# Performance work log

Hardware: AMD Instinct MI355X
Metric: run time of the kernel (lower is better)

The kernel has to match this reference:

```python
import jax, jax.numpy as jnp
import numpy as np

B, S, D, H = 4, 2048, 1024, 16
HD = D // H

def setup_inputs() -> dict:
    key = jax.random.key(0)
    ks = jax.random.split(key, 12)
    std = 1.0 / np.sqrt(D)
    inp = {
        'query': jax.random.normal(ks[0], (B, S, D), jnp.float32),
        'key':   jax.random.normal(ks[1], (B, S, D), jnp.float32),
        'value': jax.random.normal(ks[2], (B, S, D), jnp.float32),
        'mask':  jnp.tril(jnp.ones((S, S), jnp.int32))[None, None, :, :],  # [1,1,S,S] causal
        'Wq': jax.random.uniform(ks[3], (D, D), jnp.float32, -std, std),
        'bq': jax.random.uniform(ks[4], (D,), jnp.float32, -std, std),
        'Wk': jax.random.uniform(ks[5], (D, D), jnp.float32, -std, std),
        'bk': jax.random.uniform(ks[6], (D,), jnp.float32, -std, std),
        'Wv': jax.random.uniform(ks[7], (D, D), jnp.float32, -std, std),
        'bv': jax.random.uniform(ks[8], (D,), jnp.float32, -std, std),
        'Wo': jax.random.uniform(ks[9], (D, D), jnp.float32, -std, std),
        'bo': jax.random.uniform(ks[10], (D,), jnp.float32, -std, std),
    }
    return inp

def _split_heads(x, W, b):
    # torch Linear: x @ W.T + b ; then [B,S,H,HD] -> [B,H,S,HD]
    y = jnp.einsum('bsd,ed->bse', x, W) + b
    return y.reshape(x.shape[0], -1, H, HD).transpose(0, 2, 1, 3)

def reference(query, key, value, mask, Wq, bq, Wk, bk, Wv, bv, Wo, bo):
    q = _split_heads(query, Wq, bq)   # [B,H,S,HD]
    k = _split_heads(key,   Wk, bk)
    v = _split_heads(value, Wv, bv)
    logits = jnp.einsum('bhqd,bhkd->bhqk', q, k) / np.sqrt(HD)  # [B,H,S,S]
    logits = jnp.where(mask == 0, jnp.float32(-1e9), logits)
    attn = jax.nn.softmax(logits, axis=-1)
    out = jnp.einsum('bhqk,bhkd->bhqd', attn, v)               # [B,H,S,HD]
    out = out.transpose(0, 2, 1, 3).reshape(query.shape[0], -1, D)
    return jnp.einsum('bsd,ed->bse', out, Wo) + bo
```

## Files before the change

kernel.cpp:

```cpp
#include <hip/hip_runtime.h>
#include <hip/hip_bf16.h>


#define SLEN 2048
#define DMOD 1024

typedef __attribute__((ext_vector_type(8))) short s16x8;
typedef __attribute__((ext_vector_type(4))) float f32x4;

__device__ __forceinline__ unsigned short f2bf(float f) {
    union { __hip_bfloat16 h; unsigned short u; } cv;
    cv.h = __float2bfloat16(f);
    return cv.u;
}
__device__ __forceinline__ unsigned cvtpk(float a, float b) {
    unsigned r;
    asm("v_cvt_pk_bf16_f32 %0, %1, %2" : "=v"(r) : "v"(a), "v"(b));
    return r;
}
__device__ __forceinline__ void gload_lds16(const void* g, void* l) {
    __builtin_amdgcn_global_load_lds(
        (const __attribute__((address_space(1))) void*)g,
        (__attribute__((address_space(3))) void*)l, 16, 0, 0);
}

__global__ __launch_bounds__(256) void convert_w(
    const float* __restrict__ wq, const float* __restrict__ wk,
    const float* __restrict__ wv, const float* __restrict__ wo,
    unsigned short* __restrict__ dst)
{
    const int bid = blockIdx.x, tid = threadIdx.x;
    const int w = bid >> 7;
    const float* src = (w == 0) ? wq : (w == 1) ? wk : (w == 2) ? wv : wo;
    unsigned short* d = dst + (size_t)w * 1048576;
    const size_t off = (size_t)(bid & 127) * 8192;
#pragma unroll
    for (int i = 0; i < 8; ++i) {
        const size_t e = off + (size_t)(i * 256 + tid) * 4;
        float4 x = *reinterpret_cast<const float4*>(&src[e]);
        uint2 u;
        u.x = cvtpk(x.x, x.y);
        u.y = cvtpk(x.z, x.w);
        *reinterpret_cast<uint2*>(&d[e]) = u;
    }
}

template<int MODE>
__global__ __launch_bounds__(256, 2) void gemm_qkv(
    const float* __restrict__ A, const unsigned short* __restrict__ W,
    const float* __restrict__ bias, unsigned short* __restrict__ outp,
    float oscale)
{
    __shared__ unsigned short Asm[2][8192];
    __shared__ unsigned short Bsm[2][8192];

    const int tid  = threadIdx.x;
    const int lane = tid & 63, wid = tid >> 6;
    const int l15 = lane & 15, lhi = lane >> 4;

    const int flat = blockIdx.x;
    const int logical = (flat & 7) * 64 + (flat >> 3);
    const int m0 = (logical >> 3) * 128, n0 = (logical & 7) * 128;
    const int wr = wid >> 1, wc = wid & 1;

    int soff[4];
    const float* aptc[4];
#pragma unroll
    for (int i = 0; i < 4; ++i) {
        const int f = i * 256 + tid;
        const int srow = f >> 3, sg = f & 7;
        soff[i] = srow * 128 + ((sg ^ (srow & 7)) * 16);
        aptc[i] = A + (size_t)(m0 + srow) * 1024 + sg * 8;
    }
    const int wsrow = lane >> 3;
    const int wsgr  = (lane & 7) ^ wsrow;
    const unsigned short* bpt = W + (size_t)(n0 + wid * 8 + wsrow) * 1024 + wsgr * 8;

    int aoff[2][4], boff[2][4];
#pragma unroll
    for (int kk = 0; kk < 2; ++kk)
#pragma unroll
        for (int i = 0; i < 4; ++i) {
            const int s = ((4 * kk + lhi) ^ (l15 & 7)) * 16;
            aoff[kk][i] = (wr * 64 + i * 16 + l15) * 128 + s;
            boff[kk][i] = (wc * 64 + i * 16 + l15) * 128 + s;
        }

    f32x4 acc[4][4];
#pragma unroll
    for (int i = 0; i < 4; ++i)
#pragma unroll
        for (int j = 0; j < 4; ++j) acc[i][j] = (f32x4)0.f;

    float4 awE[8], awO[8];

    auto loadTo = [&](float4 (&aw)[8], int k0) {
#pragma unroll
        for (int i = 0; i < 4; ++i) {
            aw[2 * i]     = *reinterpret_cast<const float4*>(aptc[i] + k0);
            aw[2 * i + 1] = *reinterpret_cast<const float4*>(aptc[i] + k0 + 4);
        }
    };
    auto writeFrom = [&](float4 (&aw)[8], int bsel) {
#pragma unroll
        for (int i = 0; i < 4; ++i) {
            uint4 u;
            u.x = cvtpk(aw[2 * i].x,     aw[2 * i].y);
            u.y = cvtpk(aw[2 * i].z,     aw[2 * i].w);
            u.z = cvtpk(aw[2 * i + 1].x, aw[2 * i + 1].y);
            u.w = cvtpk(aw[2 * i + 1].z, aw[2 * i + 1].w);
            *reinterpret_cast<uint4*>((char*)&Asm[bsel][0] + soff[i]) = u;
        }
    };
    auto stageW = [&](int bsel) {
        char* bd = (char*)Bsm + bsel * 16384 + wid * 1024;
#pragma unroll
        for (int i = 0; i < 4; ++i)
            gload_lds16(bpt + i * 32768, bd + i * 4096);
        bpt += 64;
    };
    auto mfmaPhase = [&](const char* AB, const char* BB) {
#pragma unroll
        for (int kk = 0; kk < 2; ++kk) {
            s16x8 af[4], bfv[4];
#pragma unroll
            for (int i = 0; i < 4; ++i) af[i]  = *reinterpret_cast<const s16x8*>(AB + aoff[kk][i]);
#pragma unroll
            for (int j = 0; j < 4; ++j) bfv[j] = *reinterpret_cast<const s16x8*>(BB + boff[kk][j]);
#pragma unroll
            for (int i = 0; i < 4; ++i)
#pragma unroll
                for (int j = 0; j < 4; ++j)
                    acc[i][j] = __builtin_amdgcn_mfma_f32_16x16x32_bf16(af[i], bfv[j], acc[i][j], 0, 0, 0);
        }
    };
    auto barrier8 = [&]() {
        asm volatile("s_waitcnt vmcnt(8) lgkmcnt(0)" ::: "memory");
        __builtin_amdgcn_s_barrier();
        __builtin_amdgcn_sched_barrier(0);
    };
    auto barrier0 = [&]() {
        asm volatile("s_waitcnt vmcnt(0) lgkmcnt(0)" ::: "memory");
        __builtin_amdgcn_s_barrier();
        __builtin_amdgcn_sched_barrier(0);
    };

    loadTo(awE, 0);
    stageW(0);
    writeFrom(awE, 0);
    loadTo(awO, 64);
    barrier8();

#pragma unroll 1
    for (int kt = 0; kt < 16; kt += 2) {
        if (kt + 1 < 16) stageW(1);
        if (kt + 2 < 16) loadTo(awE, (kt + 2) * 64);
        mfmaPhase((const char*)&Asm[0][0], (const char*)&Bsm[0][0]);
        if (kt + 1 < 16) writeFrom(awO, 1);
        if (kt + 2 < 16) barrier8(); else barrier0();
        if (kt + 2 < 16) stageW(0);
        if (kt + 3 < 16) loadTo(awO, (kt + 3) * 64);
        mfmaPhase((const char*)&Asm[1][0], (const char*)&Bsm[1][0]);
        if (kt + 2 < 16) writeFrom(awE, 0);
        if (kt + 3 < 16) barrier8(); else barrier0();
    }

#pragma unroll
    for (int j = 0; j < 4; ++j) {
        const int col = n0 + wc * 64 + j * 16 + l15;
        const float bv = bias[col];
#pragma unroll
        for (int i = 0; i < 4; ++i) {
#pragma unroll
            for (int r = 0; r < 4; ++r) {
                const int row = m0 + wr * 64 + i * 16 + lhi * 4 + r;
                const float val = (acc[i][j][r] + bv) * oscale;
                if constexpr (MODE == 0) {
                    outp[(size_t)((row >> 11) * 16 + (col >> 6)) * 131072
                         + (size_t)(row & 2047) * 64 + (col & 63)] = f2bf(val);
                } else {
                    outp[(size_t)((row >> 11) * 16 + (col >> 6)) * 131072
                         + (size_t)(col & 63) * 2048 + (row & 2047)] = f2bf(val);
                }
            }
        }
    }
}

__global__ __launch_bounds__(256) void gemm_out(
    const unsigned short* __restrict__ A, const unsigned short* __restrict__ W,
    const float* __restrict__ bias, float* __restrict__ outp)
{
    __shared__ unsigned short Asm[2][8192];
    __shared__ unsigned short Bsm[2][8192];

    const int tid  = threadIdx.x;
    const int lane = tid & 63, wid = tid >> 6;
    const int l15 = lane & 15, lhi = lane >> 4;

    const int flat = blockIdx.x;
    const int logical = (flat & 7) * 64 + (flat >> 3);
    const int m0 = (logical >> 3) * 128, n0 = (logical & 7) * 128;

    const int wr = wid >> 1, wc = wid & 1;
    const int srow = lane >> 3;
    const int sgr  = (lane & 7) ^ srow;

    int aoff[2][4], boff[2][4];
#pragma unroll
    for (int kk = 0; kk < 2; ++kk)
#pragma unroll
        for (int i = 0; i < 4; ++i) {
            const int s = ((4 * kk + lhi) ^ (l15 & 7)) * 16;
            aoff[kk][i] = (wr * 64 + i * 16 + l15) * 128 + s;
            boff[kk][i] = (wc * 64 + i * 16 + l15) * 128 + s;
        }

    const unsigned short* apt = A + (size_t)(m0 + wid * 8 + srow) * 1024 + sgr * 8;
    const unsigned short* bpt = W + (size_t)(n0 + wid * 8 + srow) * 1024 + sgr * 8;

    f32x4 acc[4][4];
#pragma unroll
    for (int i = 0; i < 4; ++i)
#pragma unroll
        for (int j = 0; j < 4; ++j) acc[i][j] = (f32x4)0.f;

    auto stage = [&](int bsel) {
        char* ad = (char*)Asm + bsel * 16384 + wid * 1024;
        char* bd = (char*)Bsm + bsel * 16384 + wid * 1024;
#pragma unroll
        for (int i = 0; i < 4; ++i) {
            gload_lds16(apt + i * 32768, ad + i * 4096);
            gload_lds16(bpt + i * 32768, bd + i * 4096);
        }
        apt += 64; bpt += 64;
    };

    stage(0);
    __syncthreads();
    int cur = 0;
#pragma unroll 1
    for (int kt = 0; kt < 16; ++kt) {
        if (kt < 15) stage(cur ^ 1);
        const char* AB = (const char*)Asm + cur * 16384;
        const char* BB = (const char*)Bsm + cur * 16384;
#pragma unroll
        for (int kk = 0; kk < 2; ++kk) {
            s16x8 af[4], bfv[4];
#pragma unroll
            for (int i = 0; i < 4; ++i) af[i]  = *reinterpret_cast<const s16x8*>(AB + aoff[kk][i]);
#pragma unroll
            for (int j = 0; j < 4; ++j) bfv[j] = *reinterpret_cast<const s16x8*>(BB + boff[kk][j]);
#pragma unroll
            for (int i = 0; i < 4; ++i)
#pragma unroll
                for (int j = 0; j < 4; ++j)
                    acc[i][j] = __builtin_amdgcn_mfma_f32_16x16x32_bf16(af[i], bfv[j], acc[i][j], 0, 0, 0);
        }
        __syncthreads();
        cur ^= 1;
    }

#pragma unroll
    for (int j = 0; j < 4; ++j) {
        const int col = n0 + wc * 64 + j * 16 + l15;
        const float bv = bias[col];
#pragma unroll
        for (int i = 0; i < 4; ++i)
#pragma unroll
            for (int r = 0; r < 4; ++r) {
                const int row = m0 + wr * 64 + i * 16 + lhi * 4 + r;
                outp[(size_t)row * 1024 + col] = acc[i][j][r] + bv;
            }
    }
}

#define EXPC 0.18033688011112043f

__global__ __launch_bounds__(256, 4) void attn_kernel(
    const unsigned short* __restrict__ Q,
    const unsigned short* __restrict__ Kc,
    const unsigned short* __restrict__ Vt,
    unsigned short* __restrict__ Ao)
{
    __shared__ char smem[40960];

    const int tid = threadIdx.x, lane = tid & 63, wid = tid >> 6;
    const int l15 = lane & 15, lhi = lane >> 4;
    const int sK = l15 & 7;
    const int sub = lane >> 3, c8s = lane & 7;
    const int thr = wid * 16 + l15;

    const int kb0 = l15 * 128 + (lhi ^ sK) * 16;
    const int kb1 = kb0 ^ 64;
    char* const pb0 = smem + 32768 + wid * 2048 + kb0;
    char* const pb1 = smem + 32768 + wid * 2048 + kb1;
    char* const PWp = smem + 32768 + wid * 2048;
    int pw[4];
#pragma unroll
    for (int nb = 0; nb < 4; ++nb)
        pw[nb] = (l15 * 16 + ((nb * 4 + lhi) ^ (2 * sK))) * 8;

    const int flat = blockIdx.x;
    const int logical = (flat & 7) * 128 + (flat >> 3);
    const int bx = logical & 15, bh = logical >> 4;
    const int qtL = bx, qtH = 31 - bx;
    const int q0L = qtL * 64, q0H = qtH * 64;

    const size_t base = (size_t)bh * SLEN * 64;
    const unsigned short* Qb = Q + base;
    const unsigned short* Kb = Kc + base;
    const unsigned short* Vb = Vt + base;
    const int b = bh >> 4, h = bh & 15;
    const int scol = (c8s ^ sub) * 8;

    const f32x4 fzero = (f32x4)0.f;
    const s16x8 onesb = (s16x8)(short)0x3F80;

    s16x8 aqL[2], aqH[2];
#pragma unroll
    for (int kk = 0; kk < 2; ++kk) {
        aqL[kk] = *reinterpret_cast<const s16x8*>(
            &Qb[(size_t)(q0L + wid * 16 + l15) * 64 + kk * 32 + 8 * lhi]);
        aqH[kk] = *reinterpret_cast<const s16x8*>(
            &Qb[(size_t)(q0H + wid * 16 + l15) * 64 + kk * 32 + 8 * lhi]);
    }

    f32x4 oL[4], oH[4];
#pragma unroll
    for (int nb = 0; nb < 4; ++nb) { oL[nb] = (f32x4)0.f; oH[nb] = (f32x4)0.f; }
    f32x4 lL = (f32x4)0.f, lH = (f32x4)0.f;

    const unsigned short* kpt = Kb + (16 * wid + sub) * 64 + scol;
    const unsigned short* vpt = Vb + (size_t)(16 * wid + sub) * SLEN + scol;

    auto stage = [&](int bsel) {
        char* kd = smem + bsel * 8192 + wid * 2048;
        char* vd = smem + 16384 + bsel * 8192 + wid * 2048;
        gload_lds16(kpt,         kd);
        gload_lds16(kpt + 512,   kd + 1024);
        gload_lds16(vpt,         vd);
        gload_lds16(vpt + 16384, vd + 1024);
        kpt += 4096; vpt += 64;
    };

    auto tile = [&](s16x8 (&aq)[2], f32x4 (&o_acc)[4], f32x4& l_acc,
                    bool domask, const char* c0, const char* c1) {
        f32x4 sc2[4];
        __builtin_amdgcn_s_setprio(1);
        {
            s16x8 ak[4];
#pragma unroll
            for (int nb = 0; nb < 4; ++nb)
                ak[nb] = *reinterpret_cast<const s16x8*>(c0 + nb * 2048);
#pragma unroll
            for (int nb = 0; nb < 4; ++nb)
                sc2[nb] = __builtin_amdgcn_mfma_f32_16x16x32_bf16(ak[nb], aq[0], fzero, 0, 0, 0);
#pragma unroll
            for (int nb = 0; nb < 4; ++nb)
                ak[nb] = *reinterpret_cast<const s16x8*>(c1 + nb * 2048);
#pragma unroll
            for (int nb = 0; nb < 4; ++nb)
                sc2[nb] = __builtin_amdgcn_mfma_f32_16x16x32_bf16(ak[nb], aq[1], sc2[nb], 0, 0, 0);
        }
        __builtin_amdgcn_s_setprio(0);

        if (domask) {
#pragma unroll
            for (int nb = 0; nb < 4; ++nb)
#pragma unroll
                for (int r = 0; r < 4; ++r)
                    if (nb * 16 + lhi * 4 + r > thr) sc2[nb][r] = -1e30f;
        }

#pragma unroll
        for (int nb = 0; nb < 4; ++nb) {
            float p0 = exp2f(sc2[nb][0]);
            float p1 = exp2f(sc2[nb][1]);
            float p2 = exp2f(sc2[nb][2]);
            float p3 = exp2f(sc2[nb][3]);
            uint2 u;
            u.x = cvtpk(p0, p1);
            u.y = cvtpk(p2, p3);
            *reinterpret_cast<uint2*>(PWp + pw[nb]) = u;
        }

        __builtin_amdgcn_s_setprio(1);
#pragma unroll
        for (int kk = 0; kk < 2; ++kk) {
            s16x8 pa = *reinterpret_cast<const s16x8*>(kk ? pb1 : pb0);
            const char* vb = (kk ? c1 : c0) + 16384;
            s16x8 bvv[4];
#pragma unroll
            for (int nb = 0; nb < 4; ++nb)
                bvv[nb] = *reinterpret_cast<const s16x8*>(vb + nb * 2048);
#pragma unroll
            for (int nb = 0; nb < 4; ++nb)
                o_acc[nb] = __builtin_amdgcn_mfma_f32_16x16x32_bf16(pa, bvv[nb], o_acc[nb], 0, 0, 0);
            l_acc = __builtin_amdgcn_mfma_f32_16x16x32_bf16(pa, onesb, l_acc, 0, 0, 0);
        }
        __builtin_amdgcn_s_setprio(0);
    };

    stage(0);
    __syncthreads();
    int cur = 0;
    const int nt = qtH + 1;

#pragma unroll 1
    for (int t = 0; t < nt; ++t) {
        if (t + 1 < nt) stage(cur ^ 1);
        const char* c0 = smem + cur * 8192 + kb0;
        const char* c1 = smem + cur * 8192 + kb1;
        if (t <= qtL) tile(aqL, oL, lL, t == qtL, c0, c1);
        tile(aqH, oH, lH, t == qtH, c0, c1);
        __syncthreads();
        cur ^= 1;
    }

    float liL[4], liH[4];
#pragma unroll
    for (int r = 0; r < 4; ++r) { liL[r] = 1.0f / lL[r]; liH[r] = 1.0f / lH[r]; }
#pragma unroll
    for (int nb = 0; nb < 4; ++nb)
#pragma unroll
        for (int r = 0; r < 4; ++r) {
            const int sL = q0L + wid * 16 + lhi * 4 + r;
            const int sH = q0H + wid * 16 + lhi * 4 + r;
            const size_t cix = h * 64 + nb * 16 + l15;
            Ao[((size_t)b * SLEN + sL) * DMOD + cix] = f2bf(oL[nb][r] * liL[r]);
            Ao[((size_t)b * SLEN + sH) * DMOD + cix] = f2bf(oH[nb][r] * liH[r]);
        }
}

extern "C" void kernel_launch(void* const* d_in, const int* in_sizes, int n_in,
                              void* d_out, int out_size, void* d_ws, size_t ws_size,
                              hipStream_t stream) {
    const float* q  = (const float*)d_in[0];
    const float* k  = (const float*)d_in[1];
    const float* v  = (const float*)d_in[2];
    const float* Wq = (const float*)d_in[4];
    const float* bq = (const float*)d_in[5];
    const float* Wk = (const float*)d_in[6];
    const float* bk = (const float*)d_in[7];
    const float* Wv = (const float*)d_in[8];
    const float* bv = (const float*)d_in[9];
    const float* Wo = (const float*)d_in[10];
    const float* bo = (const float*)d_in[11];

    unsigned short* wsp = (unsigned short*)d_ws;
    unsigned short* wqc = wsp;
    unsigned short* wkc = wsp + 1048576;
    unsigned short* wvc = wsp + 2097152;
    unsigned short* woc = wsp + 3145728;
    unsigned short* qb  = wsp + 4194304;
    unsigned short* kb  = wsp + 12582912;
    unsigned short* vtb = wsp + 20971520;
    unsigned short* ao  = wsp + 29360128;

    dim3 gb(256);
    convert_w<<<dim3(512), gb, 0, stream>>>(Wq, Wk, Wv, Wo, wsp);
    gemm_qkv<0><<<dim3(512), gb, 0, stream>>>(q, wqc, bq, qb, EXPC);
    gemm_qkv<0><<<dim3(512), gb, 0, stream>>>(k, wkc, bk, kb, 1.0f);
    gemm_qkv<1><<<dim3(512), gb, 0, stream>>>(v, wvc, bv, vtb, 1.0f);
    attn_kernel<<<dim3(1024), gb, 0, stream>>>(qb, kb, vtb, ao);
    gemm_out<<<dim3(512), gb, 0, stream>>>(ao, woc, bo, (float*)d_out);
}
```

Baseline: 170.3 us.

## Single-buffer V tile in LDS to raise occupancy to five blocks

Shrinks the attention kernel's shared memory from 40 KB to 32 KB by keeping only one V buffer, so launch bounds can be raised from four to five blocks per CU. V for the current tile is loaded at the start of each iteration and waited on with explicit vmcnt waits and a barrier between the QK/softmax phase and the PV phase, while K stays double-buffered. This uses manual waitcnt/barrier synchronisation instead of __syncthreads. The gain in occupancy is paid for with an extra barrier per iteration and V load latency that is now exposed. The tighter launch bound may also force register spills.

```diff
diff --git a/kernel.cpp b/kernel.cpp
--- a/kernel.cpp
+++ b/kernel.cpp
@@ -277,13 +277,13 @@
 
 #define EXPC 0.18033688011112043f
 
-__global__ __launch_bounds__(256, 4) void attn_kernel(
+__global__ __launch_bounds__(256, 5) void attn_kernel(
     const unsigned short* __restrict__ Q,
     const unsigned short* __restrict__ Kc,
     const unsigned short* __restrict__ Vt,
     unsigned short* __restrict__ Ao)
 {
-    __shared__ char smem[40960];
+    __shared__ char smem[32768];
 
     const int tid = threadIdx.x, lane = tid & 63, wid = tid >> 6;
     const int l15 = lane & 15, lhi = lane >> 4;
@@ -293,9 +293,11 @@
 
     const int kb0 = l15 * 128 + (lhi ^ sK) * 16;
     const int kb1 = kb0 ^ 64;
-    char* const pb0 = smem + 32768 + wid * 2048 + kb0;
-    char* const pb1 = smem + 32768 + wid * 2048 + kb1;
-    char* const PWp = smem + 32768 + wid * 2048;
+    char* const pb0 = smem + 24576 + wid * 2048 + kb0;
+    char* const pb1 = smem + 24576 + wid * 2048 + kb1;
+    char* const PWp = smem + 24576 + wid * 2048;
+    const char* const vr0 = smem + 16384 + kb0;
+    const char* const vr1 = smem + 16384 + kb1;
     int pw[4];
 #pragma unroll
     for (int nb = 0; nb < 4; ++nb)
@@ -334,18 +336,20 @@
     const unsigned short* kpt = Kb + (16 * wid + sub) * 64 + scol;
     const unsigned short* vpt = Vb + (size_t)(16 * wid + sub) * SLEN + scol;
 
-    auto stage = [&](int bsel) {
+    auto stageK = [&](int bsel) {
         char* kd = smem + bsel * 8192 + wid * 2048;
-        char* vd = smem + 16384 + bsel * 8192 + wid * 2048;
-        gload_lds16(kpt,         kd);
-        gload_lds16(kpt + 512,   kd + 1024);
+        gload_lds16(kpt,       kd);
+        gload_lds16(kpt + 512, kd + 1024);
+        kpt += 4096;
+    };
+    auto stageV = [&]() {
+        char* vd = smem + 16384 + wid * 2048;
         gload_lds16(vpt,         vd);
         gload_lds16(vpt + 16384, vd + 1024);
-        kpt += 4096; vpt += 64;
-    };
-
-    auto tile = [&](s16x8 (&aq)[2], f32x4 (&o_acc)[4], f32x4& l_acc,
-                    bool domask, const char* c0, const char* c1) {
+        vpt += 64;
+    };
+
+    auto qksm = [&](s16x8 (&aq)[2], bool domask, const char* c0, const char* c1) {
         f32x4 sc2[4];
         __builtin_amdgcn_s_setprio(1);
         {
@@ -372,7 +376,6 @@
                 for (int r = 0; r < 4; ++r)
                     if (nb * 16 + lhi * 4 + r > thr) sc2[nb][r] = -1e30f;
         }
-
 #pragma unroll
         for (int nb = 0; nb < 4; ++nb) {
             float p0 = exp2f(sc2[nb][0]);
@@ -384,12 +387,14 @@
             u.y = cvtpk(p2, p3);
             *reinterpret_cast<uint2*>(PWp + pw[nb]) = u;
         }
-
+    };
+
+    auto pv = [&](f32x4 (&o_acc)[4], f32x4& l_acc) {
         __builtin_amdgcn_s_setprio(1);
 #pragma unroll
         for (int kk = 0; kk < 2; ++kk) {
             s16x8 pa = *reinterpret_cast<const s16x8*>(kk ? pb1 : pb0);
-            const char* vb = (kk ? c1 : c0) + 16384;
+            const char* vb = kk ? vr1 : vr0;
             s16x8 bvv[4];
 #pragma unroll
             for (int nb = 0; nb < 4; ++nb)
@@ -402,19 +407,43 @@
         __builtin_amdgcn_s_setprio(0);
     };
 
-    stage(0);
-    __syncthreads();
+    stageK(0);
+    asm volatile("s_waitcnt vmcnt(0)" ::: "memory");
+    __builtin_amdgcn_s_barrier();
+    __builtin_amdgcn_sched_barrier(0);
+
     int cur = 0;
     const int nt = qtH + 1;
 
 #pragma unroll 1
     for (int t = 0; t < nt; ++t) {
-        if (t + 1 < nt) stage(cur ^ 1);
+        stageV();
+        const bool pk = (t + 1 < nt);
+        if (pk) stageK(cur ^ 1);
         const char* c0 = smem + cur * 8192 + kb0;
         const char* c1 = smem + cur * 8192 + kb1;
-        if (t <= qtL) tile(aqL, oL, lL, t == qtL, c0, c1);
-        tile(aqH, oH, lH, t == qtH, c0, c1);
-        __syncthreads();
+
+        if (t <= qtL) {
+            qksm(aqL, t == qtL, c0, c1);
+            if (pk) asm volatile("s_waitcnt vmcnt(2)" ::: "memory");
+            else    asm volatile("s_waitcnt vmcnt(0)" ::: "memory");
+            __builtin_amdgcn_s_barrier();
+            __builtin_amdgcn_sched_barrier(0);
+            pv(oL, lL);
+            qksm(aqH, false, c0, c1);
+            pv(oH, lH);
+        } else {
+            qksm(aqH, t == qtH, c0, c1);
+            if (pk) asm volatile("s_waitcnt vmcnt(2)" ::: "memory");
+            else    asm volatile("s_waitcnt vmcnt(0)" ::: "memory");
+            __builtin_amdgcn_s_barrier();
+            __builtin_amdgcn_sched_barrier(0);
+            pv(oH, lH);
+        }
+
+        asm volatile("s_waitcnt vmcnt(0) lgkmcnt(0)" ::: "memory");
+        __builtin_amdgcn_s_barrier();
+        __builtin_amdgcn_sched_barrier(0);
         cur ^= 1;
     }
 
```

Measured after the change: 486.0 us. 185% more time.
